# Performance work log

Measured on AMD Instinct MI355X. Metric: run time of the kernel, lower is better.

Reference implementation:

```python
import math
import jax, jax.numpy as jnp
import numpy as np

B, T, C, H, TOP_K = 2, 2048, 1024, 16, 256
D = C // H  # head_dim = 64


def setup_inputs() -> dict:
    key = jax.random.key(0)
    kx, kq, kk, kv, ko = jax.random.split(key, 5)
    s = 1.0 / math.sqrt(C)
    return {
        "x": jax.random.normal(kx, (B, T, C), dtype=jnp.float32),
        "Wq": jax.random.normal(kq, (C, C), dtype=jnp.float32) * s,
        "Wk": jax.random.normal(kk, (C, C), dtype=jnp.float32) * s,
        "Wv": jax.random.normal(kv, (C, C), dtype=jnp.float32) * s,
        "Wo": jax.random.normal(ko, (C, C), dtype=jnp.float32) * s,
    }


def _sparsify_last_dim_topk(x, keep_k):
    # keep the keep_k largest-|.| entries along the last dim, zero the rest
    a = jnp.abs(x)
    kth = jax.lax.top_k(a, keep_k)[0][..., -1:]  # k-th largest magnitude
    return jnp.where(a >= kth, x, jnp.zeros_like(x))


def reference(x, Wq, Wk, Wv, Wo):
    b, t, c = x.shape
    k_keep = min(TOP_K, t)

    def proj(W):  # nn.Linear (no bias): x @ W.T, then split heads -> [B,H,T,D]
        return (x @ W.T).reshape(b, t, H, D).transpose(0, 2, 1, 3)

    q, k, v = proj(Wq), proj(Wk), proj(Wv)

    # feature-dim sparsification: keep ratio = k_keep / T of head_dim features
    feat_keep = max(1, math.ceil(D * k_keep / t))
    q = _sparsify_last_dim_topk(q, feat_keep)
    k = _sparsify_last_dim_topk(k, feat_keep)
    v = _sparsify_last_dim_topk(v, feat_keep)

    scores = jnp.einsum("bhtd,bhsd->bhts", q, k) / math.sqrt(D)  # [B,H,T,T]
    causal = jnp.tril(jnp.ones((t, t), dtype=bool))  # True = visible
    neg_inf = jnp.float32(-jnp.inf)
    scores = jnp.where(causal, scores, neg_inf)

    # row-wise top-k: keep k_keep largest scores per query row, -inf elsewhere
    kth = jax.lax.top_k(scores, k_keep)[0][..., -1:]
    sparse_scores = jnp.where(scores >= kth, scores, neg_inf)

    attn = jax.nn.softmax(sparse_scores, axis=-1)  # dropout p=0 (eval)
    out = jnp.einsum("bhts,bhsd->bhtd", attn, v)
    out = out.transpose(0, 2, 1, 3).reshape(b, t, c)
    return out @ Wo.T
```

## Files before the change

### kernel.cpp

```cpp
#include <hip/hip_runtime.h>
#include <cstdint>

constexpr int Tn = 2048;
constexpr int Cn = 1024;
constexpr int Mn = 4096;
constexpr int KKEEP = 256;
constexpr int FKEEP = 8;
constexpr unsigned U_NEG_INF = 0x007FFFFFu;

constexpr int NW     = 4;
constexpr int NJMAX  = 32;

__device__ __forceinline__ unsigned umap(float f) {
    unsigned b = __float_as_uint(f);
    return (b & 0x80000000u) ? ~b : (b | 0x80000000u);
}
__device__ __forceinline__ float uunmap(unsigned u) {
    return __uint_as_float((u & 0x80000000u) ? (u ^ 0x80000000u) : ~u);
}

__device__ __forceinline__ unsigned short f2bf(float f) {
    unsigned u = __float_as_uint(f);
    u += 0x7FFFu + ((u >> 16) & 1u);
    return (unsigned short)(u >> 16);
}
struct bfpair { unsigned short h, l; };
__device__ __forceinline__ bfpair split_bf16(float x) {
    bfpair r;
    r.h = f2bf(x);
    r.l = f2bf(x - __uint_as_float((unsigned)r.h << 16));
    return r;
}

__device__ __forceinline__ int   rli(int v, int l)   { return __builtin_amdgcn_readlane(v, l); }
__device__ __forceinline__ float rlf(float v, int l) {
    return __int_as_float(__builtin_amdgcn_readlane(__float_as_int(v), l));
}

typedef __attribute__((ext_vector_type(8))) short          short8v;
typedef __attribute__((ext_vector_type(8))) unsigned short ushort8v;
typedef __attribute__((ext_vector_type(4))) float          f32x4;

constexpr size_t XCHUNK = (size_t)Mn * Cn / 8;
constexpr size_t WCHUNK = (size_t)Cn * Cn / 8;
constexpr size_t WELEMS = (size_t)Cn * Cn;

__device__ __forceinline__ void split8(const float* s, unsigned short* dh,
                                       unsigned short* dl, size_t base)
{
    const float4 a = *(const float4*)&s[base], b = *(const float4*)&s[base + 4];
    ushort8v h, l; bfpair p;
    p = split_bf16(a.x); h[0] = p.h; l[0] = p.l;
    p = split_bf16(a.y); h[1] = p.h; l[1] = p.l;
    p = split_bf16(a.z); h[2] = p.h; l[2] = p.l;
    p = split_bf16(a.w); h[3] = p.h; l[3] = p.l;
    p = split_bf16(b.x); h[4] = p.h; l[4] = p.l;
    p = split_bf16(b.y); h[5] = p.h; l[5] = p.l;
    p = split_bf16(b.z); h[6] = p.h; l[6] = p.l;
    p = split_bf16(b.w); h[7] = p.h; l[7] = p.l;
    *(ushort8v*)&dh[base] = h;
    *(ushort8v*)&dl[base] = l;
}

__global__ __launch_bounds__(256)
void presplit(const float* __restrict__ x,  const float* __restrict__ Wq,
              const float* __restrict__ Wk, const float* __restrict__ Wv,
              unsigned short* __restrict__ XH, unsigned short* __restrict__ XL,
              unsigned short* __restrict__ WHL)
{
    const size_t cid = (size_t)blockIdx.x * 256 + threadIdx.x;
    if (cid < XCHUNK) {
        split8(x, XH, XL, cid * 8);
    } else {
        const size_t c2 = cid - XCHUNK;
        const int    z  = (int)(c2 / WCHUNK);
        const size_t e  = (c2 % WCHUNK) * 8;
        const float* src = (z == 0) ? Wq : (z == 1 ? Wk : Wv);
        unsigned short* dh = WHL + (size_t)z * 2 * WELEMS;
        unsigned short* dl = dh + WELEMS;
        split8(src, dh, dl, e);
    }
}

__global__ __launch_bounds__(256, 2)
void gemm_qkv_ps(const unsigned short* __restrict__ XH,
                 const unsigned short* __restrict__ XL,
                 const unsigned short* __restrict__ WHL,
                 float* __restrict__ O0, float* __restrict__ O1,
                 float* __restrict__ O2)
{
    const int z = blockIdx.z;
    const unsigned short* WH = WHL + (size_t)z * 2 * WELEMS;
    const unsigned short* WL = WH + WELEMS;
    float* O = (z == 0) ? O0 : (z == 1 ? O1 : O2);

    __shared__ unsigned short Ah[128][40], Al[128][40];
    __shared__ unsigned short Bh[128][40], Bl[128][40];

    const int tid  = threadIdx.x;
    const int lane = tid & 63;
    const int wv   = tid >> 6;
    const int wm   = wv >> 1, wn = wv & 1;
    const int fm   = lane & 15;
    const int fq   = lane >> 4;
    const int m0   = blockIdx.y * 128;
    const int n0   = blockIdx.x * 128;

    f32x4 acc[4][4] = {};

    for (int k0 = 0; k0 < Cn; k0 += 32) {
        __syncthreads();
#pragma unroll
        for (int r = 0; r < 2; ++r) {
            const int idx = tid + r * 256;
            const int row = idx >> 2, c8 = (idx & 3) * 8;
            const size_t ao = (size_t)(m0 + row) * Cn + k0 + c8;
            const size_t bo = (size_t)(n0 + row) * Cn + k0 + c8;
            *(ushort8v*)&Ah[row][c8] = *(const ushort8v*)&XH[ao];
            *(ushort8v*)&Al[row][c8] = *(const ushort8v*)&XL[ao];
            *(ushort8v*)&Bh[row][c8] = *(const ushort8v*)&WH[bo];
            *(ushort8v*)&Bl[row][c8] = *(const ushort8v*)&WL[bo];
        }
        __syncthreads();

        short8v ah[4], al[4], bh[4], bl[4];
#pragma unroll
        for (int ti = 0; ti < 4; ++ti) {
            ah[ti] = *(const short8v*)&Ah[wm * 64 + ti * 16 + fm][fq * 8];
            al[ti] = *(const short8v*)&Al[wm * 64 + ti * 16 + fm][fq * 8];
            bh[ti] = *(const short8v*)&Bh[wn * 64 + ti * 16 + fm][fq * 8];
            bl[ti] = *(const short8v*)&Bl[wn * 64 + ti * 16 + fm][fq * 8];
        }
#pragma unroll
        for (int ti = 0; ti < 4; ++ti)
#pragma unroll
            for (int tj = 0; tj < 4; ++tj) {
                acc[ti][tj] = __builtin_amdgcn_mfma_f32_16x16x32_bf16(
                    ah[ti], bh[tj], acc[ti][tj], 0, 0, 0);
                acc[ti][tj] = __builtin_amdgcn_mfma_f32_16x16x32_bf16(
                    ah[ti], bl[tj], acc[ti][tj], 0, 0, 0);
                acc[ti][tj] = __builtin_amdgcn_mfma_f32_16x16x32_bf16(
                    al[ti], bh[tj], acc[ti][tj], 0, 0, 0);
            }
    }

#pragma unroll
    for (int ti = 0; ti < 4; ++ti)
#pragma unroll
        for (int tj = 0; tj < 4; ++tj)
#pragma unroll
            for (int r = 0; r < 4; ++r) {
                const int row = m0 + wm * 64 + ti * 16 + fq * 4 + r;
                const int col = n0 + wn * 64 + tj * 16 + fm;
                O[(size_t)row * Cn + col] = acc[ti][tj][r];
            }
}

__global__ __launch_bounds__(256, 2)
void gemm_out_ps(const unsigned short* __restrict__ AH,
                 const unsigned short* __restrict__ AL,
                 const float* __restrict__ Wo, float* __restrict__ O)
{
    __shared__ unsigned short Ah[128][40], Al[128][40];
    __shared__ unsigned short Bh[128][40], Bl[128][40];

    const int tid  = threadIdx.x;
    const int lane = tid & 63;
    const int wv   = tid >> 6;
    const int wm   = wv >> 1, wn = wv & 1;
    const int fm   = lane & 15;
    const int fq   = lane >> 4;
    const int m0   = blockIdx.y * 128;
    const int n0   = blockIdx.x * 128;

    f32x4 acc[4][4] = {};

    for (int k0 = 0; k0 < Cn; k0 += 32) {
        __syncthreads();
#pragma unroll
        for (int r = 0; r < 2; ++r) {
            const int idx = tid + r * 256;
            const int row = idx >> 2, c8 = (idx & 3) * 8;
            const size_t ao = (size_t)(m0 + row) * Cn + k0 + c8;
            *(ushort8v*)&Ah[row][c8] = *(const ushort8v*)&AH[ao];
            *(ushort8v*)&Al[row][c8] = *(const ushort8v*)&AL[ao];
            {
                const float* s = &Wo[(size_t)(n0 + row) * Cn + k0 + c8];
                const float4 x0 = *(const float4*)s, x1 = *(const float4*)(s + 4);
                ushort8v h, l;
                bfpair p;
                p = split_bf16(x0.x); h[0] = p.h; l[0] = p.l;
                p = split_bf16(x0.y); h[1] = p.h; l[1] = p.l;
                p = split_bf16(x0.z); h[2] = p.h; l[2] = p.l;
                p = split_bf16(x0.w); h[3] = p.h; l[3] = p.l;
                p = split_bf16(x1.x); h[4] = p.h; l[4] = p.l;
                p = split_bf16(x1.y); h[5] = p.h; l[5] = p.l;
                p = split_bf16(x1.z); h[6] = p.h; l[6] = p.l;
                p = split_bf16(x1.w); h[7] = p.h; l[7] = p.l;
                *(ushort8v*)&Bh[row][c8] = h;
                *(ushort8v*)&Bl[row][c8] = l;
            }
        }
        __syncthreads();

        short8v ah[4], al[4], bh[4], bl[4];
#pragma unroll
        for (int ti = 0; ti < 4; ++ti) {
            ah[ti] = *(const short8v*)&Ah[wm * 64 + ti * 16 + fm][fq * 8];
            al[ti] = *(const short8v*)&Al[wm * 64 + ti * 16 + fm][fq * 8];
            bh[ti] = *(const short8v*)&Bh[wn * 64 + ti * 16 + fm][fq * 8];
            bl[ti] = *(const short8v*)&Bl[wn * 64 + ti * 16 + fm][fq * 8];
        }
#pragma unroll
        for (int ti = 0; ti < 4; ++ti)
#pragma unroll
            for (int tj = 0; tj < 4; ++tj) {
                acc[ti][tj] = __builtin_amdgcn_mfma_f32_16x16x32_bf16(
                    ah[ti], bh[tj], acc[ti][tj], 0, 0, 0);
                acc[ti][tj] = __builtin_amdgcn_mfma_f32_16x16x32_bf16(
                    ah[ti], bl[tj], acc[ti][tj], 0, 0, 0);
                acc[ti][tj] = __builtin_amdgcn_mfma_f32_16x16x32_bf16(
                    al[ti], bh[tj], acc[ti][tj], 0, 0, 0);
            }
    }

#pragma unroll
    for (int ti = 0; ti < 4; ++ti)
#pragma unroll
        for (int tj = 0; tj < 4; ++tj)
#pragma unroll
            for (int r = 0; r < 4; ++r) {
                const int row = m0 + wm * 64 + ti * 16 + fq * 4 + r;
                const int col = n0 + wn * 64 + tj * 16 + fm;
                O[(size_t)row * Cn + col] = acc[ti][tj][r];
            }
}

__global__ __launch_bounds__(256)
void sparsify_topk(float* __restrict__ Q, float* __restrict__ V)
{
    const int wid  = (blockIdx.x * 256 + threadIdx.x) >> 6;
    const int lane = threadIdx.x & 63;
    const int tensor = wid >> 16;
    const int vec    = wid & 65535;
    float* base = tensor ? V : Q;

    const size_t off = (size_t)vec * 64 + lane;
    const float v = base[off];
    const float a = fabsf(v);

    int cnt = 0;
#pragma unroll
    for (int j = 0; j < 64; ++j) {
        const float aj = __shfl(a, j);
        cnt += (aj > a) ? 1 : 0;
    }
    float cand = (cnt < FKEEP) ? a : 3.402823466e38f;
#pragma unroll
    for (int o = 32; o; o >>= 1) cand = fminf(cand, __shfl_xor(cand, o));
    base[off] = (a >= cand) ? v : 0.0f;
}

__global__ __launch_bounds__(256)
void sparsify_k_t(const float* __restrict__ K, float* __restrict__ KT)
{
    __shared__ float tile[64][65];

    const int tid = threadIdx.x;
    const int w = tid >> 6, lane = tid & 63;
    const int tt = blockIdx.x;
    const int bh = blockIdx.y;
    const int b = bh >> 4, h = bh & 15;
    const int t0 = tt * 64;

#pragma unroll
    for (int k = 0; k < 4; ++k) {
        const int c = tid + k * 256;
        const int row = c >> 4, off = (c & 15) * 4;
        const float4 v4 = *(const float4*)
            &K[(size_t)((b * Tn + t0 + row) * 16 + h) * 64 + off];
        tile[row][off + 0] = v4.x; tile[row][off + 1] = v4.y;
        tile[row][off + 2] = v4.z; tile[row][off + 3] = v4.w;
    }
    __syncthreads();

#pragma unroll 1
    for (int r = w; r < 64; r += 4) {
        const float v = tile[r][lane];
        const float a = fabsf(v);
        int cnt = 0;
#pragma unroll
        for (int j = 0; j < 64; ++j) {
            const float aj = __shfl(a, j);
            cnt += (aj > a) ? 1 : 0;
        }
        float cand = (cnt < FKEEP) ? a : 3.402823466e38f;
#pragma unroll
        for (int o = 32; o; o >>= 1) cand = fminf(cand, __shfl_xor(cand, o));
        tile[r][lane] = (a >= cand) ? v : 0.0f;
    }
    __syncthreads();

#pragma unroll
    for (int k = 0; k < 16; ++k) {
        const int d = w + k * 4;
        KT[(((size_t)bh * 64 + d) << 11) + t0 + lane] = tile[lane][d];
    }
}

__global__ __launch_bounds__(256, 4)
void attn_kernel(const float* __restrict__ Qm, const float* __restrict__ KTm,
                 const float* __restrict__ Vm,
                 unsigned short* __restrict__ AOH,
                 unsigned short* __restrict__ AOL)
{
    __shared__ unsigned hist[NW * 256];
    __shared__ unsigned ctab[NW * 256];
    __shared__ unsigned ptab[NW * 256];

    const int tid  = threadIdx.x;
    const int w    = tid >> 6;
    const int lane = tid & 63;
    const int bh   = blockIdx.y;
    const int b    = bh >> 4;
    const int h    = bh & 15;
    const int t    = blockIdx.x * NW + w;
    const size_t rowoff = ((size_t)(b * Tn + t) << 10) + (h << 6);
    const size_t kvoff  = ((size_t)(b * Tn) << 10) + (h << 6);

    const float q0  = Qm[rowoff + lane];
    const float qsc = q0 * 0.125f;
    const unsigned long long nzm = __ballot(q0 != 0.0f);
    const int nnz = __popcll(nzm);

    const int nj = (t >> 6) + 1;
    const float* ktb = KTm + ((size_t)bh << 17);

    const bool dosel = (t >= KKEEP);
    unsigned* hrow = hist + w * 256;
    hrow[lane] = 0; hrow[64 + lane] = 0; hrow[128 + lane] = 0; hrow[192 + lane] = 0;
    __asm__ volatile("s_waitcnt lgkmcnt(0)" ::: "memory");

    unsigned sv[NJMAX];
    unsigned rowmax = 0u;
    if (nnz == 8) {
        float mq[8]; int moff[8];
        {
            unsigned long long mm = nzm;
#pragma unroll
            for (int i = 0; i < 8; ++i) {
                const int m = (int)__builtin_ctzll(mm); mm &= mm - 1;
                mq[i] = rlf(qsc, m);
                moff[i] = m << 11;
            }
        }
#pragma unroll
        for (int jq = 0; jq < NJMAX / 4; ++jq) {
            const int j0 = jq * 4;
            if (j0 >= nj) {
                sv[j0] = U_NEG_INF; sv[j0 + 1] = U_NEG_INF;
                sv[j0 + 2] = U_NEG_INF; sv[j0 + 3] = U_NEG_INF;
                continue;
            }
            const int c0 = (j0 << 6) + lane;
            if (j0 + 4 <= nj) {
                float s0 = 0.0f, s1 = 0.0f, s2 = 0.0f, s3 = 0.0f;
#pragma unroll
                for (int i = 0; i < 8; ++i) {
                    const float* kpi = ktb + moff[i];
                    s0 += mq[i] * kpi[c0];
                    s1 += mq[i] * kpi[c0 + 64];
                    s2 += mq[i] * kpi[c0 + 128];
                    s3 += mq[i] * kpi[c0 + 192];
                }
                const unsigned v0 = (c0       <= t) ? umap(s0) : U_NEG_INF;
                const unsigned v1 = (c0 +  64 <= t) ? umap(s1) : U_NEG_INF;
                const unsigned v2 = (c0 + 128 <= t) ? umap(s2) : U_NEG_INF;
                const unsigned v3 = (c0 + 192 <= t) ? umap(s3) : U_NEG_INF;
                sv[j0] = v0; sv[j0 + 1] = v1; sv[j0 + 2] = v2; sv[j0 + 3] = v3;
                unsigned m01 = (v0 > v1) ? v0 : v1;
                unsigned m23 = (v2 > v3) ? v2 : v3;
                m01 = (m01 > m23) ? m01 : m23;
                rowmax = (m01 > rowmax) ? m01 : rowmax;
                if (dosel) {
                    atomicAdd(&hrow[v0 >> 24], 1u);
                    atomicAdd(&hrow[v1 >> 24], 1u);
                    atomicAdd(&hrow[v2 >> 24], 1u);
                    atomicAdd(&hrow[v3 >> 24], 1u);
                }
            } else {
#pragma unroll
                for (int k = 0; k < 4; ++k) {
                    const int j = j0 + k;
                    if (j < nj) {
                        const int col = (j << 6) + lane;
                        float s = 0.0f;
#pragma unroll
                        for (int i = 0; i < 8; ++i)
                            s += mq[i] * ktb[moff[i] + col];
                        const unsigned v = (col <= t) ? umap(s) : U_NEG_INF;
                        sv[j] = v;
                        rowmax = (v > rowmax) ? v : rowmax;
                        if (dosel) atomicAdd(&hrow[v >> 24], 1u);
                    } else sv[j] = U_NEG_INF;
                }
            }
        }
    } else {
#pragma unroll
        for (int j = 0; j < NJMAX; ++j) {
            if (j >= nj) { sv[j] = U_NEG_INF; continue; }
            const int col = (j << 6) + lane;
            float s = 0.0f;
            unsigned long long mm = nzm;
            while (mm) {
                const int m = (int)__builtin_ctzll(mm); mm &= mm - 1;
                s += rlf(qsc, m) * ktb[((size_t)m << 11) + col];
            }
            const unsigned val = (col <= t) ? umap(s) : U_NEG_INF;
            sv[j] = val;
            rowmax = (val > rowmax) ? val : rowmax;
            if (dosel) atomicAdd(&hrow[val >> 24], 1u);
        }
    }

#pragma unroll
    for (int o = 32; o; o >>= 1) {
        const unsigned m2 = __shfl_xor(rowmax, o);
        rowmax = (m2 > rowmax) ? m2 : rowmax;
    }
    const float fm = uunmap(rowmax);

    unsigned cur = U_NEG_INF;
    if (dosel) {
        unsigned prefix = 0u, pmask = 0u;
        unsigned r = KKEEP;
#pragma unroll 1
        for (int level = 0; level < 4; ++level) {
            const int sh = 24 - 8 * level;
            if (level) {
                hrow[lane] = 0; hrow[64 + lane] = 0;
                hrow[128 + lane] = 0; hrow[192 + lane] = 0;
                __asm__ volatile("s_waitcnt lgkmcnt(0)" ::: "memory");
#pragma unroll
                for (int j = 0; j < NJMAX; ++j) {
                    if (j < nj) {
                        const int col = (j << 6) + lane;
                        const unsigned v = sv[j];
                        if (col <= t && (v & pmask) == prefix)
                            atomicAdd(&hrow[(v >> sh) & 255u], 1u);
                    }
                }
            }
            __asm__ volatile("s_waitcnt lgkmcnt(0)" ::: "memory");
            const uint4 hv = *(const uint4*)&hrow[lane * 4];
            const unsigned ls = hv.x + hv.y + hv.z + hv.w;
            unsigned sfx = ls;
#pragma unroll
            for (int off = 1; off < 64; off <<= 1) {
                const unsigned tt2 = __shfl_down(sfx, off);
                if (lane + off < 64) sfx += tt2;
            }
            const unsigned excl = sfx - ls;
            const unsigned c3 = excl + hv.w, c2 = c3 + hv.z,
                           c1 = c2 + hv.y,  c0 = c1 + hv.x;
            int bsel = -1; unsigned csel = 0, cnext = 0;
            if      (c3 >= r) { bsel = 4 * lane + 3; csel = c3; cnext = excl; }
            else if (c2 >= r) { bsel = 4 * lane + 2; csel = c2; cnext = c3; }
            else if (c1 >= r) { bsel = 4 * lane + 1; csel = c1; cnext = c2; }
            else if (c0 >= r) { bsel = 4 * lane + 0; csel = c0; cnext = c1; }
            int B = bsel;
#pragma unroll
            for (int off = 32; off; off >>= 1) {
                const int ob = __shfl_xor(B, off);
                B = (ob > B) ? ob : B;
            }
            const unsigned cB  = (unsigned)__shfl((int)csel,  B >> 2);
            const unsigned cB1 = (unsigned)__shfl((int)cnext, B >> 2);
            prefix |= (unsigned)B << sh;
            pmask  |= 255u << sh;
            if (cB == r || level == 3) { cur = prefix; break; }
            r -= cB1;
        }
    }

    unsigned* ct = ctab + w * 256;
    unsigned* cp = ptab + w * 256;
    float ps = 0.0f;
    int cnt = 0; bool ovf = false;
#pragma unroll
    for (int j = 0; j < NJMAX; ++j) {
        if (j >= nj) continue;
        const int col = (j << 6) + lane;
        float pv = 0.0f;
        const unsigned uv = sv[j];
        if (col <= t && uv >= cur) pv = __expf(uunmap(uv) - fm);
        ps += pv;
        const unsigned long long m = __ballot(pv > 0.0f);
        const int c = __popcll(m);
        if (cnt + c <= 256) {
            if (pv > 0.0f) {
                const int pos = cnt + __popcll(m & ((1ull << lane) - 1ull));
                ct[pos] = (unsigned)col;
                cp[pos] = __float_as_uint(pv);
            }
        } else ovf = true;
        cnt += c;
    }
#pragma unroll
    for (int o = 32; o; o >>= 1) ps += __shfl_xor(ps, o);
    const float inv = 1.0f / ps;

    if (!ovf) {
        int   cR[4]; float pR[4];
#pragma unroll
        for (int blk = 0; blk < 4; ++blk) {
            const int idx = blk * 64 + lane;
            cR[blk] = (idx < cnt) ? (int)ct[idx] : 0;
            pR[blk] = (idx < cnt) ? __uint_as_float(cp[idx]) : 0.0f;
        }
        const int g  = lane >> 4;
        const int d0 = (lane & 15) * 4;
        float ax = 0.0f, ay = 0.0f, az = 0.0f, aw = 0.0f;
        const float* __restrict__ vb4 = Vm + kvoff + d0;
        auto do_blk = [&](int blk_c, float blk_p) {
#pragma unroll
            for (int j = 0; j < 16; ++j) {
                const int   c = __shfl(blk_c, 4 * j + g);
                const float p = __shfl(blk_p, 4 * j + g);
                const float4 v4 = *(const float4*)&vb4[(size_t)c * Cn];
                ax += p * v4.x; ay += p * v4.y;
                az += p * v4.z; aw += p * v4.w;
            }
        };
        do_blk(cR[0], pR[0]);
        if (cnt > 64)  do_blk(cR[1], pR[1]);
        if (cnt > 128) do_blk(cR[2], pR[2]);
        if (cnt > 192) do_blk(cR[3], pR[3]);
#pragma unroll
        for (int o = 16; o <= 32; o <<= 1) {
            ax += __shfl_xor(ax, o);
            ay += __shfl_xor(ay, o);
            az += __shfl_xor(az, o);
            aw += __shfl_xor(aw, o);
        }
        if (g == 0) {
            const float vx = ax * inv, vy = ay * inv,
                        vz = az * inv, vw = aw * inv;
            const bfpair px = split_bf16(vx), py = split_bf16(vy),
                         pz = split_bf16(vz), pw = split_bf16(vw);
            ushort4 hq, lq;
            hq.x = px.h; hq.y = py.h; hq.z = pz.h; hq.w = pw.h;
            lq.x = px.l; lq.y = py.l; lq.z = pz.l; lq.w = pw.l;
            *(ushort4*)&AOH[rowoff + d0] = hq;
            *(ushort4*)&AOL[rowoff + d0] = lq;
        }
    } else {
        const float* __restrict__ vcol = Vm + kvoff + lane;
        float acc = 0.0f;
#pragma unroll
        for (int j = 0; j < NJMAX; ++j) {
            if (j >= nj) continue;
            const int col = (j << 6) + lane;
            float pv = 0.0f;
            const unsigned uv = sv[j];
            if (col <= t && uv >= cur) pv = __expf(uunmap(uv) - fm);
            unsigned long long m = __ballot(pv > 0.0f);
            const int cb = j << 6;
            while (m) {
                const int l0 = __builtin_ctzll(m); m &= m - 1;
                const float w0 = __shfl(pv, l0);
                const float v0 = vcol[(size_t)(cb + l0) * Cn];
                float w1 = 0.0f, v1 = 0.0f;
                if (m) {
                    const int l1 = __builtin_ctzll(m); m &= m - 1;
                    w1 = __shfl(pv, l1);
                    v1 = vcol[(size_t)(cb + l1) * Cn];
                }
                acc += w0 * v0;
                acc += w1 * v1;
            }
        }
        const float v = acc * inv;
        const bfpair p = split_bf16(v);
        AOH[rowoff + lane] = p.h;
        AOL[rowoff + lane] = p.l;
    }
}

extern "C" void kernel_launch(void* const* d_in, const int* in_sizes, int n_in,
                              void* d_out, int out_size, void* d_ws, size_t ws_size,
                              hipStream_t stream)
{
    const float* x  = (const float*)d_in[0];
    const float* Wq = (const float*)d_in[1];
    const float* Wk = (const float*)d_in[2];
    const float* Wv = (const float*)d_in[3];
    const float* Wo = (const float*)d_in[4];
    float* out = (float*)d_out;

    float* Q  = (float*)d_ws;
    float* K  = Q + (size_t)Mn * Cn;
    float* V  = K + (size_t)Mn * Cn;
    float* KT = V + (size_t)Mn * Cn;

    unsigned short* XH  = (unsigned short*)d_out;
    unsigned short* XL  = XH + (size_t)Mn * Cn;
    unsigned short* WHL = (unsigned short*)KT;
    unsigned short* AOH = (unsigned short*)K;
    unsigned short* AOL = AOH + (size_t)Mn * Cn;

    presplit<<<dim3((unsigned)((XCHUNK + 3 * WCHUNK) / 256)), 256, 0, stream>>>(
        x, Wq, Wk, Wv, XH, XL, WHL);

    gemm_qkv_ps<<<dim3(Cn / 128, Mn / 128, 3), 256, 0, stream>>>(
        XH, XL, WHL, Q, K, V);

    sparsify_topk<<<dim3(2 * 65536 / 4), 256, 0, stream>>>(Q, V);

    sparsify_k_t<<<dim3(32, 32), 256, 0, stream>>>(K, KT);

    attn_kernel<<<dim3(Tn / NW, 32), 256, 0, stream>>>(Q, KT, V, AOH, AOL);

    gemm_out_ps<<<dim3(Cn / 128, Mn / 128, 1), 256, 0, stream>>>(
        AOH, AOL, Wo, out);
}
```

Before: 798.6 us.

## Pair causal rows t and T-1-t per wave to balance attention work

Each wave now handles two query rows, a short row tA and its mirror tB = T-1-tA, so every wave does about the same causal work and the grid halves. Score computation, radix top-k selection and the PV accumulation for both rows are interleaved to add memory-level parallelism. Column/probability pairs are packed into a single uint2 LDS table and read back directly instead of through shuffles. The cost is higher register pressure (48 score registers plus doubled accumulators) and twice the LDS use per block, which may lower occupancy.

```diff
diff --git a/kernel.cpp b/kernel.cpp
--- a/kernel.cpp
+++ b/kernel.cpp
@@ -8,8 +8,9 @@
 constexpr int FKEEP = 8;
 constexpr unsigned U_NEG_INF = 0x007FFFFFu;
 
-constexpr int NW     = 4;
-constexpr int NJMAX  = 32;
+constexpr int NW  = 4;
+constexpr int NJA = 16;
+constexpr int NJB = 32;
 
 __device__ __forceinline__ unsigned umap(float f) {
     unsigned b = __float_as_uint(f);
@@ -314,9 +315,8 @@
                  unsigned short* __restrict__ AOH,
                  unsigned short* __restrict__ AOL)
 {
-    __shared__ unsigned hist[NW * 256];
-    __shared__ unsigned ctab[NW * 256];
-    __shared__ unsigned ptab[NW * 256];
+    __shared__ unsigned histA[NW * 256], histB[NW * 256];
+    __shared__ uint2    cpkA[NW * 256], cpkB[NW * 256];
 
     const int tid  = threadIdx.x;
     const int w    = tid >> 6;
@@ -324,247 +324,427 @@
     const int bh   = blockIdx.y;
     const int b    = bh >> 4;
     const int h    = bh & 15;
-    const int t    = blockIdx.x * NW + w;
-    const size_t rowoff = ((size_t)(b * Tn + t) << 10) + (h << 6);
-    const size_t kvoff  = ((size_t)(b * Tn) << 10) + (h << 6);
-
-    const float q0  = Qm[rowoff + lane];
-    const float qsc = q0 * 0.125f;
-    const unsigned long long nzm = __ballot(q0 != 0.0f);
-    const int nnz = __popcll(nzm);
-
-    const int nj = (t >> 6) + 1;
+    const int tA   = blockIdx.x * NW + w;
+    const int tB   = (Tn - 1) - tA;
+    const size_t rowoffA = ((size_t)(b * Tn + tA) << 10) + (h << 6);
+    const size_t rowoffB = ((size_t)(b * Tn + tB) << 10) + (h << 6);
+    const size_t kvoff   = ((size_t)(b * Tn) << 10) + (h << 6);
+
+    const float qA = Qm[rowoffA + lane];
+    const float qB = Qm[rowoffB + lane];
+    const float qscA = qA * 0.125f, qscB = qB * 0.125f;
+    const unsigned long long nzmA = __ballot(qA != 0.0f);
+    const unsigned long long nzmB = __ballot(qB != 0.0f);
+    const int nnzA = __popcll(nzmA), nnzB = __popcll(nzmB);
+
+    const int njA = (tA >> 6) + 1;
+    const int njB = (tB >> 6) + 1;
     const float* ktb = KTm + ((size_t)bh << 17);
 
-    const bool dosel = (t >= KKEEP);
-    unsigned* hrow = hist + w * 256;
-    hrow[lane] = 0; hrow[64 + lane] = 0; hrow[128 + lane] = 0; hrow[192 + lane] = 0;
+    const bool doselA = (tA >= KKEEP);
+    unsigned* hrowA = histA + w * 256;
+    unsigned* hrowB = histB + w * 256;
+    hrowA[lane] = 0; hrowA[64 + lane] = 0; hrowA[128 + lane] = 0; hrowA[192 + lane] = 0;
+    hrowB[lane] = 0; hrowB[64 + lane] = 0; hrowB[128 + lane] = 0; hrowB[192 + lane] = 0;
     __asm__ volatile("s_waitcnt lgkmcnt(0)" ::: "memory");
 
-    unsigned sv[NJMAX];
-    unsigned rowmax = 0u;
-    if (nnz == 8) {
-        float mq[8]; int moff[8];
+    unsigned svA[NJA], svB[NJB];
+    unsigned rmA = 0u, rmB = 0u;
+
+    if (nnzA == 8 && nnzB == 8) {
+        float mqA[8], mqB[8]; int moA[8], moB[8];
         {
-            unsigned long long mm = nzm;
+            unsigned long long mm = nzmA;
 #pragma unroll
             for (int i = 0; i < 8; ++i) {
                 const int m = (int)__builtin_ctzll(mm); mm &= mm - 1;
-                mq[i] = rlf(qsc, m);
-                moff[i] = m << 11;
-            }
-        }
-#pragma unroll
-        for (int jq = 0; jq < NJMAX / 4; ++jq) {
+                mqA[i] = rlf(qscA, m); moA[i] = m << 11;
+            }
+        }
+        {
+            unsigned long long mm = nzmB;
+#pragma unroll
+            for (int i = 0; i < 8; ++i) {
+                const int m = (int)__builtin_ctzll(mm); mm &= mm - 1;
+                mqB[i] = rlf(qscB, m); moB[i] = m << 11;
+            }
+        }
+#pragma unroll
+        for (int jq = 0; jq < 8; ++jq) {
             const int j0 = jq * 4;
-            if (j0 >= nj) {
-                sv[j0] = U_NEG_INF; sv[j0 + 1] = U_NEG_INF;
-                sv[j0 + 2] = U_NEG_INF; sv[j0 + 3] = U_NEG_INF;
-                continue;
-            }
-            const int c0 = (j0 << 6) + lane;
-            if (j0 + 4 <= nj) {
-                float s0 = 0.0f, s1 = 0.0f, s2 = 0.0f, s3 = 0.0f;
-#pragma unroll
-                for (int i = 0; i < 8; ++i) {
-                    const float* kpi = ktb + moff[i];
-                    s0 += mq[i] * kpi[c0];
-                    s1 += mq[i] * kpi[c0 + 64];
-                    s2 += mq[i] * kpi[c0 + 128];
-                    s3 += mq[i] * kpi[c0 + 192];
-                }
-                const unsigned v0 = (c0       <= t) ? umap(s0) : U_NEG_INF;
-                const unsigned v1 = (c0 +  64 <= t) ? umap(s1) : U_NEG_INF;
-                const unsigned v2 = (c0 + 128 <= t) ? umap(s2) : U_NEG_INF;
-                const unsigned v3 = (c0 + 192 <= t) ? umap(s3) : U_NEG_INF;
-                sv[j0] = v0; sv[j0 + 1] = v1; sv[j0 + 2] = v2; sv[j0 + 3] = v3;
-                unsigned m01 = (v0 > v1) ? v0 : v1;
-                unsigned m23 = (v2 > v3) ? v2 : v3;
-                m01 = (m01 > m23) ? m01 : m23;
-                rowmax = (m01 > rowmax) ? m01 : rowmax;
-                if (dosel) {
-                    atomicAdd(&hrow[v0 >> 24], 1u);
-                    atomicAdd(&hrow[v1 >> 24], 1u);
-                    atomicAdd(&hrow[v2 >> 24], 1u);
-                    atomicAdd(&hrow[v3 >> 24], 1u);
+            if (j0 < njB) {
+                const int c0 = (j0 << 6) + lane;
+                if (j0 + 4 <= njB) {
+                    float s0 = 0, s1 = 0, s2 = 0, s3 = 0;
+#pragma unroll
+                    for (int i = 0; i < 8; ++i) {
+                        const float* kp = ktb + moB[i];
+                        s0 += mqB[i] * kp[c0];
+                        s1 += mqB[i] * kp[c0 + 64];
+                        s2 += mqB[i] * kp[c0 + 128];
+                        s3 += mqB[i] * kp[c0 + 192];
+                    }
+                    const unsigned v0 = (c0       <= tB) ? umap(s0) : U_NEG_INF;
+                    const unsigned v1 = (c0 +  64 <= tB) ? umap(s1) : U_NEG_INF;
+                    const unsigned v2 = (c0 + 128 <= tB) ? umap(s2) : U_NEG_INF;
+                    const unsigned v3 = (c0 + 192 <= tB) ? umap(s3) : U_NEG_INF;
+                    svB[j0] = v0; svB[j0 + 1] = v1; svB[j0 + 2] = v2; svB[j0 + 3] = v3;
+                    unsigned m01 = (v0 > v1) ? v0 : v1;
+                    unsigned m23 = (v2 > v3) ? v2 : v3;
+                    m01 = (m01 > m23) ? m01 : m23;
+                    rmB = (m01 > rmB) ? m01 : rmB;
+                    atomicAdd(&hrowB[v0 >> 24], 1u);
+                    atomicAdd(&hrowB[v1 >> 24], 1u);
+                    atomicAdd(&hrowB[v2 >> 24], 1u);
+                    atomicAdd(&hrowB[v3 >> 24], 1u);
+                } else {
+#pragma unroll
+                    for (int k = 0; k < 4; ++k) {
+                        const int j = j0 + k;
+                        if (j < njB) {
+                            const int col = (j << 6) + lane;
+                            float s = 0;
+#pragma unroll
+                            for (int i = 0; i < 8; ++i) s += mqB[i] * ktb[moB[i] + col];
+                            const unsigned v = (col <= tB) ? umap(s) : U_NEG_INF;
+                            svB[j] = v;
+                            rmB = (v > rmB) ? v : rmB;
+                            atomicAdd(&hrowB[v >> 24], 1u);
+                        } else svB[j] = U_NEG_INF;
+                    }
                 }
             } else {
-#pragma unroll
-                for (int k = 0; k < 4; ++k) {
-                    const int j = j0 + k;
-                    if (j < nj) {
-                        const int col = (j << 6) + lane;
-                        float s = 0.0f;
-#pragma unroll
-                        for (int i = 0; i < 8; ++i)
-                            s += mq[i] * ktb[moff[i] + col];
-                        const unsigned v = (col <= t) ? umap(s) : U_NEG_INF;
-                        sv[j] = v;
-                        rowmax = (v > rowmax) ? v : rowmax;
-                        if (dosel) atomicAdd(&hrow[v >> 24], 1u);
-                    } else sv[j] = U_NEG_INF;
+                svB[j0] = U_NEG_INF; svB[j0 + 1] = U_NEG_INF;
+                svB[j0 + 2] = U_NEG_INF; svB[j0 + 3] = U_NEG_INF;
+            }
+            if (jq < 4) {
+                if (j0 < njA) {
+                    const int c0 = (j0 << 6) + lane;
+                    if (j0 + 4 <= njA) {
+                        float s0 = 0, s1 = 0, s2 = 0, s3 = 0;
+#pragma unroll
+                        for (int i = 0; i < 8; ++i) {
+                            const float* kp = ktb + moA[i];
+                            s0 += mqA[i] * kp[c0];
+                            s1 += mqA[i] * kp[c0 + 64];
+                            s2 += mqA[i] * kp[c0 + 128];
+                            s3 += mqA[i] * kp[c0 + 192];
+                        }
+                        const unsigned v0 = (c0       <= tA) ? umap(s0) : U_NEG_INF;
+                        const unsigned v1 = (c0 +  64 <= tA) ? umap(s1) : U_NEG_INF;
+                        const unsigned v2 = (c0 + 128 <= tA) ? umap(s2) : U_NEG_INF;
+                        const unsigned v3 = (c0 + 192 <= tA) ? umap(s3) : U_NEG_INF;
+                        svA[j0] = v0; svA[j0 + 1] = v1; svA[j0 + 2] = v2; svA[j0 + 3] = v3;
+                        unsigned m01 = (v0 > v1) ? v0 : v1;
+                        unsigned m23 = (v2 > v3) ? v2 : v3;
+                        m01 = (m01 > m23) ? m01 : m23;
+                        rmA = (m01 > rmA) ? m01 : rmA;
+                        if (doselA) {
+                            atomicAdd(&hrowA[v0 >> 24], 1u);
+                            atomicAdd(&hrowA[v1 >> 24], 1u);
+                            atomicAdd(&hrowA[v2 >> 24], 1u);
+                            atomicAdd(&hrowA[v3 >> 24], 1u);
+                        }
+                    } else {
+#pragma unroll
+                        for (int k = 0; k < 4; ++k) {
+                            const int j = j0 + k;
+                            if (j < njA) {
+                                const int col = (j << 6) + lane;
+                                float s = 0;
+#pragma unroll
+                                for (int i = 0; i < 8; ++i) s += mqA[i] * ktb[moA[i] + col];
+                                const unsigned v = (col <= tA) ? umap(s) : U_NEG_INF;
+                                svA[j] = v;
+                                rmA = (v > rmA) ? v : rmA;
+                                if (doselA) atomicAdd(&hrowA[v >> 24], 1u);
+                            } else svA[j] = U_NEG_INF;
+                        }
+                    }
+                } else {
+                    svA[j0] = U_NEG_INF; svA[j0 + 1] = U_NEG_INF;
+                    svA[j0 + 2] = U_NEG_INF; svA[j0 + 3] = U_NEG_INF;
                 }
             }
         }
     } else {
 #pragma unroll
-        for (int j = 0; j < NJMAX; ++j) {
-            if (j >= nj) { sv[j] = U_NEG_INF; continue; }
+        for (int j = 0; j < NJA; ++j) {
+            if (j >= njA) { svA[j] = U_NEG_INF; continue; }
             const int col = (j << 6) + lane;
             float s = 0.0f;
-            unsigned long long mm = nzm;
+            unsigned long long mm = nzmA;
             while (mm) {
                 const int m = (int)__builtin_ctzll(mm); mm &= mm - 1;
-                s += rlf(qsc, m) * ktb[((size_t)m << 11) + col];
-            }
-            const unsigned val = (col <= t) ? umap(s) : U_NEG_INF;
-            sv[j] = val;
-            rowmax = (val > rowmax) ? val : rowmax;
-            if (dosel) atomicAdd(&hrow[val >> 24], 1u);
+                s += rlf(qscA, m) * ktb[((size_t)m << 11) + col];
+            }
+            const unsigned v = (col <= tA) ? umap(s) : U_NEG_INF;
+            svA[j] = v;
+            rmA = (v > rmA) ? v : rmA;
+            if (doselA) atomicAdd(&hrowA[v >> 24], 1u);
+        }
+#pragma unroll
+        for (int j = 0; j < NJB; ++j) {
+            if (j >= njB) { svB[j] = U_NEG_INF; continue; }
+            const int col = (j << 6) + lane;
+            float s = 0.0f;
+            unsigned long long mm = nzmB;
+            while (mm) {
+                const int m = (int)__builtin_ctzll(mm); mm &= mm - 1;
+                s += rlf(qscB, m) * ktb[((size_t)m << 11) + col];
+            }
+            const unsigned v = (col <= tB) ? umap(s) : U_NEG_INF;
+            svB[j] = v;
+            rmB = (v > rmB) ? v : rmB;
+            atomicAdd(&hrowB[v >> 24], 1u);
         }
     }
 
 #pragma unroll
     for (int o = 32; o; o >>= 1) {
-        const unsigned m2 = __shfl_xor(rowmax, o);
-        rowmax = (m2 > rowmax) ? m2 : rowmax;
-    }
-    const float fm = uunmap(rowmax);
-
-    unsigned cur = U_NEG_INF;
-    if (dosel) {
-        unsigned prefix = 0u, pmask = 0u;
-        unsigned r = KKEEP;
+        const unsigned a2 = __shfl_xor(rmA, o);
+        const unsigned b2 = __shfl_xor(rmB, o);
+        rmA = (a2 > rmA) ? a2 : rmA;
+        rmB = (b2 > rmB) ? b2 : rmB;
+    }
+    const float fmA = uunmap(rmA), fmB = uunmap(rmB);
+
+    unsigned curA = U_NEG_INF, curB = U_NEG_INF;
+    {
+        bool actA = doselA, actB = true;
+        unsigned prefA = 0u, pmaA = 0u, rA = KKEEP;
+        unsigned prefB = 0u, pmaB = 0u, rB = KKEEP;
 #pragma unroll 1
         for (int level = 0; level < 4; ++level) {
             const int sh = 24 - 8 * level;
             if (level) {
-                hrow[lane] = 0; hrow[64 + lane] = 0;
-                hrow[128 + lane] = 0; hrow[192 + lane] = 0;
+                if (actA) { hrowA[lane] = 0; hrowA[64 + lane] = 0;
+                            hrowA[128 + lane] = 0; hrowA[192 + lane] = 0; }
+                if (actB) { hrowB[lane] = 0; hrowB[64 + lane] = 0;
+                            hrowB[128 + lane] = 0; hrowB[192 + lane] = 0; }
                 __asm__ volatile("s_waitcnt lgkmcnt(0)" ::: "memory");
-#pragma unroll
-                for (int j = 0; j < NJMAX; ++j) {
-                    if (j < nj) {
-                        const int col = (j << 6) + lane;
-                        const unsigned v = sv[j];
-                        if (col <= t && (v & pmask) == prefix)
-                            atomicAdd(&hrow[(v >> sh) & 255u], 1u);
+                if (actA) {
+#pragma unroll
+                    for (int j = 0; j < NJA; ++j) {
+                        if (j < njA) {
+                            const int col = (j << 6) + lane;
+                            const unsigned v = svA[j];
+                            if (col <= tA && (v & pmaA) == prefA)
+                                atomicAdd(&hrowA[(v >> sh) & 255u], 1u);
+                        }
                     }
                 }
+                if (actB) {
+#pragma unroll
+                    for (int j = 0; j < NJB; ++j) {
+                        if (j < njB) {
+                            const int col = (j << 6) + lane;
+                            const unsigned v = svB[j];
+                            if (col <= tB && (v & pmaB) == prefB)
+                                atomicAdd(&hrowB[(v >> sh) & 255u], 1u);
+                        }
+                    }
+                }
             }
             __asm__ volatile("s_waitcnt lgkmcnt(0)" ::: "memory");
-            const uint4 hv = *(const uint4*)&hrow[lane * 4];
-            const unsigned ls = hv.x + hv.y + hv.z + hv.w;
-            unsigned sfx = ls;
-#pragma unroll
-            for (int off = 1; off < 64; off <<= 1) {
-                const unsigned tt2 = __shfl_down(sfx, off);
-                if (lane + off < 64) sfx += tt2;
-            }
-            const unsigned excl = sfx - ls;
-            const unsigned c3 = excl + hv.w, c2 = c3 + hv.z,
-                           c1 = c2 + hv.y,  c0 = c1 + hv.x;
-            int bsel = -1; unsigned csel = 0, cnext = 0;
-            if      (c3 >= r) { bsel = 4 * lane + 3; csel = c3; cnext = excl; }
-            else if (c2 >= r) { bsel = 4 * lane + 2; csel = c2; cnext = c3; }
-            else if (c1 >= r) { bsel = 4 * lane + 1; csel = c1; cnext = c2; }
-            else if (c0 >= r) { bsel = 4 * lane + 0; csel = c0; cnext = c1; }
-            int B = bsel;
-#pragma unroll
-            for (int off = 32; off; off >>= 1) {
-                const int ob = __shfl_xor(B, off);
-                B = (ob > B) ? ob : B;
-            }
-            const unsigned cB  = (unsigned)__shfl((int)csel,  B >> 2);
-            const unsigned cB1 = (unsigned)__shfl((int)cnext, B >> 2);
-            prefix |= (unsigned)B << sh;
-            pmask  |= 255u << sh;
-            if (cB == r || level == 3) { cur = prefix; break; }
-            r -= cB1;
-        }
-    }
-
-    unsigned* ct = ctab + w * 256;
-    unsigned* cp = ptab + w * 256;
-    float ps = 0.0f;
-    int cnt = 0; bool ovf = false;
-#pragma unroll
-    for (int j = 0; j < NJMAX; ++j) {
-        if (j >= nj) continue;
-        const int col = (j << 6) + lane;
-        float pv = 0.0f;
-        const unsigned uv = sv[j];
-        if (col <= t && uv >= cur) pv = __expf(uunmap(uv) - fm);
-        ps += pv;
-        const unsigned long long m = __ballot(pv > 0.0f);
-        const int c = __popcll(m);
-        if (cnt + c <= 256) {
-            if (pv > 0.0f) {
-                const int pos = cnt + __popcll(m & ((1ull << lane) - 1ull));
-                ct[pos] = (unsigned)col;
-                cp[pos] = __float_as_uint(pv);
-            }
-        } else ovf = true;
-        cnt += c;
-    }
-#pragma unroll
-    for (int o = 32; o; o >>= 1) ps += __shfl_xor(ps, o);
-    const float inv = 1.0f / ps;
-
-    if (!ovf) {
-        int   cR[4]; float pR[4];
+            if (actA) {
+                const uint4 hv = *(const uint4*)&hrowA[lane * 4];
+                const unsigned ls = hv.x + hv.y + hv.z + hv.w;
+                unsigned sfx = ls;
+#pragma unroll
+                for (int off = 1; off < 64; off <<= 1) {
+                    const unsigned tt2 = __shfl_down(sfx, off);
+                    if (lane + off < 64) sfx += tt2;
+                }
+                const unsigned excl = sfx - ls;
+                const unsigned c3 = excl + hv.w, c2 = c3 + hv.z,
+                               c1 = c2 + hv.y,  c0 = c1 + hv.x;
+                int bsel = -1; unsigned csel = 0, cnext = 0;
+                if      (c3 >= rA) { bsel = 4 * lane + 3; csel = c3; cnext = excl; }
+                else if (c2 >= rA) { bsel = 4 * lane + 2; csel = c2; cnext = c3; }
+                else if (c1 >= rA) { bsel = 4 * lane + 1; csel = c1; cnext = c2; }
+                else if (c0 >= rA) { bsel = 4 * lane + 0; csel = c0; cnext = c1; }
+                int B = bsel;
+#pragma unroll
+                for (int off = 32; off; off >>= 1) {
+                    const int ob = __shfl_xor(B, off);
+                    B = (ob > B) ? ob : B;
+                }
+                const unsigned cB  = (unsigned)__shfl((int)csel,  B >> 2);
+                const unsigned cB1 = (unsigned)__shfl((int)cnext, B >> 2);
+                prefA |= (unsigned)B << sh;
+                pmaA  |= 255u << sh;
+                if (cB == rA || level == 3) { curA = prefA; actA = false; }
+                else rA -= cB1;
+            }
+            if (actB) {
+                const uint4 hv = *(const uint4*)&hrowB[lane * 4];
+                const unsigned ls = hv.x + hv.y + hv.z + hv.w;
+                unsigned sfx = ls;
+#pragma unroll
+                for (int off = 1; off < 64; off <<= 1) {
+                    const unsigned tt2 = __shfl_down(sfx, off);
+                    if (lane + off < 64) sfx += tt2;
+                }
+                const unsigned excl = sfx - ls;
+                const unsigned c3 = excl + hv.w, c2 = c3 + hv.z,
+                               c1 = c2 + hv.y,  c0 = c1 + hv.x;
+                int bsel = -1; unsigned csel = 0, cnext = 0;
+                if      (c3 >= rB) { bsel = 4 * lane + 3; csel = c3; cnext = excl; }
+                else if (c2 >= rB) { bsel = 4 * lane + 2; csel = c2; cnext = c3; }
+                else if (c1 >= rB) { bsel = 4 * lane + 1; csel = c1; cnext = c2; }
+                else if (c0 >= rB) { bsel = 4 * lane + 0; csel = c0; cnext = c1; }
+                int B = bsel;
+#pragma unroll
+                for (int off = 32; off; off >>= 1) {
+                    const int ob = __shfl_xor(B, off);
+                    B = (ob > B) ? ob : B;
+                }
+                const unsigned cB  = (unsigned)__shfl((int)csel,  B >> 2);
+                const unsigned cB1 = (unsigned)__shfl((int)cnext, B >> 2);
+                prefB |= (unsigned)B << sh;
+                pmaB  |= 255u << sh;
+                if (cB == rB || level == 3) { curB = prefB; actB = false; }
+                else rB -= cB1;
+            }
+            if (!actA && !actB) break;
+        }
+    }
+
+    uint2* cpA = cpkA + w * 256;
+    uint2* cpB = cpkB + w * 256;
+    float invA, invB;
+    int cntA = 0, cntB = 0;
+    bool ovfA = false, ovfB = false;
+    {
+        float ps = 0.0f; int cnt = 0;
+#pragma unroll
+        for (int j = 0; j < NJA; ++j) {
+            if (j >= njA) continue;
+            const int col = (j << 6) + lane;
+            float pv = 0.0f;
+            const unsigned uv = svA[j];
+            if (col <= tA && uv >= curA) pv = __expf(uunmap(uv) - fmA);
+            ps += pv;
+            const unsigned long long m = __ballot(pv > 0.0f);
+            const int c = __popcll(m);
+            if (cnt + c <= 256) {
+                if (pv > 0.0f) {
+                    const int pos = cnt + __popcll(m & ((1ull << lane) - 1ull));
+                    cpA[pos] = make_uint2((unsigned)col, __float_as_uint(pv));
+                }
+            } else ovfA = true;
+            cnt += c;
+        }
+#pragma unroll
+        for (int o = 32; o; o >>= 1) ps += __shfl_xor(ps, o);
+        invA = 1.0f / ps; cntA = cnt;
 #pragma unroll
         for (int blk = 0; blk < 4; ++blk) {
             const int idx = blk * 64 + lane;
-            cR[blk] = (idx < cnt) ? (int)ct[idx] : 0;
-            pR[blk] = (idx < cnt) ? __uint_as_float(cp[idx]) : 0.0f;
-        }
-        const int g  = lane >> 4;
-        const int d0 = (lane & 15) * 4;
-        float ax = 0.0f, ay = 0.0f, az = 0.0f, aw = 0.0f;
-        const float* __restrict__ vb4 = Vm + kvoff + d0;
-        auto do_blk = [&](int blk_c, float blk_p) {
+            if (idx >= cntA) cpA[idx] = make_uint2(0u, 0u);
+        }
+    }
+    {
+        float ps = 0.0f; int cnt = 0;
+#pragma unroll
+        for (int j = 0; j < NJB; ++j) {
+            if (j >= njB) continue;
+            const int col = (j << 6) + lane;
+            float pv = 0.0f;
+            const unsigned uv = svB[j];
+            if (col <= tB && uv >= curB) pv = __expf(uunmap(uv) - fmB);
+            ps += pv;
+            const unsigned long long m = __ballot(pv > 0.0f);
+            const int c = __popcll(m);
+            if (cnt + c <= 256) {
+                if (pv > 0.0f) {
+                    const int pos = cnt + __popcll(m & ((1ull << lane) - 1ull));
+                    cpB[pos] = make_uint2((unsigned)col, __float_as_uint(pv));
+                }
+            } else ovfB = true;
+            cnt += c;
+        }
+#pragma unroll
+        for (int o = 32; o; o >>= 1) ps += __shfl_xor(ps, o);
+        invB = 1.0f / ps; cntB = cnt;
+#pragma unroll
+        for (int blk = 0; blk < 4; ++blk) {
+            const int idx = blk * 64 + lane;
+            if (idx >= cntB) cpB[idx] = make_uint2(0u, 0u);
+        }
+    }
+
+    const int g  = lane >> 4;
+    const int d0 = (lane & 15) * 4;
+    const float* __restrict__ vb4 = Vm + kvoff + d0;
+    float axA = 0, ayA = 0, azA = 0, awA = 0;
+    float axB = 0, ayB = 0, azB = 0, awB = 0;
+#pragma unroll
+    for (int blk = 0; blk < 4; ++blk) {
+        const bool doA = !ovfA && (cntA > blk * 64);
+        const bool doB = !ovfB && (cntB > blk * 64);
+        if (doA) {
 #pragma unroll
             for (int j = 0; j < 16; ++j) {
-                const int   c = __shfl(blk_c, 4 * j + g);
-                const float p = __shfl(blk_p, 4 * j + g);
-                const float4 v4 = *(const float4*)&vb4[(size_t)c * Cn];
-                ax += p * v4.x; ay += p * v4.y;
-                az += p * v4.z; aw += p * v4.w;
-            }
-        };
-        do_blk(cR[0], pR[0]);
-        if (cnt > 64)  do_blk(cR[1], pR[1]);
-        if (cnt > 128) do_blk(cR[2], pR[2]);
-        if (cnt > 192) do_blk(cR[3], pR[3]);
-#pragma unroll
-        for (int o = 16; o <= 32; o <<= 1) {
-            ax += __shfl_xor(ax, o);
-            ay += __shfl_xor(ay, o);
-            az += __shfl_xor(az, o);
-            aw += __shfl_xor(aw, o);
-        }
-        if (g == 0) {
-            const float vx = ax * inv, vy = ay * inv,
-                        vz = az * inv, vw = aw * inv;
-            const bfpair px = split_bf16(vx), py = split_bf16(vy),
-                         pz = split_bf16(vz), pw = split_bf16(vw);
-            ushort4 hq, lq;
-            hq.x = px.h; hq.y = py.h; hq.z = pz.h; hq.w = pw.h;
-            lq.x = px.l; lq.y = py.l; lq.z = pz.l; lq.w = pw.l;
-            *(ushort4*)&AOH[rowoff + d0] = hq;
-            *(ushort4*)&AOL[rowoff + d0] = lq;
-        }
-    } else {
+                const uint2 e = cpA[blk * 64 + 4 * j + g];
+                const float p = __uint_as_float(e.y);
+                const float4 v4 = *(const float4*)&vb4[(size_t)e.x * Cn];
+                axA += p * v4.x; ayA += p * v4.y;
+                azA += p * v4.z; awA += p * v4.w;
+            }
+        }
+        if (doB) {
+#pragma unroll
+            for (int j = 0; j < 16; ++j) {
+                const uint2 e = cpB[blk * 64 + 4 * j + g];
+                const float p = __uint_as_float(e.y);
+                const float4 v4 = *(const float4*)&vb4[(size_t)e.x * Cn];
+                axB += p * v4.x; ayB += p * v4.y;
+                azB += p * v4.z; awB += p * v4.w;
+            }
+        }
+    }
+#pragma unroll
+    for (int o = 16; o <= 32; o <<= 1) {
+        axA += __shfl_xor(axA, o); ayA += __shfl_xor(ayA, o);
+        azA += __shfl_xor(azA, o); awA += __shfl_xor(awA, o);
+        axB += __shfl_xor(axB, o); ayB += __shfl_xor(ayB, o);
+        azB += __shfl_xor(azB, o); awB += __shfl_xor(awB, o);
+    }
+    if (!ovfA && g == 0) {
+        const float vx = axA * invA, vy = ayA * invA,
+                    vz = azA * invA, vw = awA * invA;
+        const bfpair px = split_bf16(vx), py = split_bf16(vy),
+                     pz = split_bf16(vz), pw = split_bf16(vw);
+        ushort4 hq, lq;
+        hq.x = px.h; hq.y = py.h; hq.z = pz.h; hq.w = pw.h;
+        lq.x = px.l; lq.y = py.l; lq.z = pz.l; lq.w = pw.l;
+        *(ushort4*)&AOH[rowoffA + d0] = hq;
+        *(ushort4*)&AOL[rowoffA + d0] = lq;
+    }
+    if (!ovfB && g == 0) {
+        const float vx = axB * invB, vy = ayB * invB,
+                    vz = azB * invB, vw = awB * invB;
+        const bfpair px = split_bf16(vx), py = split_bf16(vy),
+                     pz = split_bf16(vz), pw = split_bf16(vw);
+        ushort4 hq, lq;
+        hq.x = px.h; hq.y = py.h; hq.z = pz.h; hq.w = pw.h;
+        lq.x = px.l; lq.y = py.l; lq.z = pz.l; lq.w = pw.l;
+        *(ushort4*)&AOH[rowoffB + d0] = hq;
+        *(ushort4*)&AOL[rowoffB + d0] = lq;
+    }
+
+    if (ovfA) {
         const float* __restrict__ vcol = Vm + kvoff + lane;
         float acc = 0.0f;
 #pragma unroll
-        for (int j = 0; j < NJMAX; ++j) {
-            if (j >= nj) continue;
+        for (int j = 0; j < NJA; ++j) {
+            if (j >= njA) continue;
             const int col = (j << 6) + lane;
             float pv = 0.0f;
-            const unsigned uv = sv[j];
-            if (col <= t && uv >= cur) pv = __expf(uunmap(uv) - fm);
+            const unsigned uv = svA[j];
+            if (col <= tA && uv >= curA) pv = __expf(uunmap(uv) - fmA);
             unsigned long long m = __ballot(pv > 0.0f);
             const int cb = j << 6;
             while (m) {
@@ -581,10 +761,41 @@
                 acc += w1 * v1;
             }
         }
-        const float v = acc * inv;
+        const float v = acc * invA;
         const bfpair p = split_bf16(v);
-        AOH[rowoff + lane] = p.h;
-        AOL[rowoff + lane] = p.l;
+        AOH[rowoffA + lane] = p.h;
+        AOL[rowoffA + lane] = p.l;
+    }
+    if (ovfB) {
+        const float* __restrict__ vcol = Vm + kvoff + lane;
+        float acc = 0.0f;
+#pragma unroll
+        for (int j = 0; j < NJB; ++j) {
+            if (j >= njB) continue;
+            const int col = (j << 6) + lane;
+            float pv = 0.0f;
+            const unsigned uv = svB[j];
+            if (col <= tB && uv >= curB) pv = __expf(uunmap(uv) - fmB);
+            unsigned long long m = __ballot(pv > 0.0f);
+            const int cb = j << 6;
+            while (m) {
+                const int l0 = __builtin_ctzll(m); m &= m - 1;
+                const float w0 = __shfl(pv, l0);
+                const float v0 = vcol[(size_t)(cb + l0) * Cn];
+                float w1 = 0.0f, v1 = 0.0f;
+                if (m) {
+                    const int l1 = __builtin_ctzll(m); m &= m - 1;
+                    w1 = __shfl(pv, l1);
+                    v1 = vcol[(size_t)(cb + l1) * Cn];
+                }
+                acc += w0 * v0;
+                acc += w1 * v1;
+            }
+        }
+        const float v = acc * invB;
+        const bfpair p = split_bf16(v);
+        AOH[rowoffB + lane] = p.h;
+        AOL[rowoffB + lane] = p.l;
     }
 }
 
@@ -620,7 +831,7 @@
 
     sparsify_k_t<<<dim3(32, 32), 256, 0, stream>>>(K, KT);
 
-    attn_kernel<<<dim3(Tn / NW, 32), 256, 0, stream>>>(Q, KT, V, AOH, AOL);
+    attn_kernel<<<dim3((Tn / 2) / NW, 32), 256, 0, stream>>>(Q, KT, V, AOH, AOL);
 
     gemm_out_ps<<<dim3(Cn / 128, Mn / 128, 1), 256, 0, stream>>>(
         AOH, AOL, Wo, out);
```

New measurement: 1.028 ms. 28.7% more time.
